# Optimization experiments

Hardware: AMD Instinct MI355X
Metric: run time of the kernel (lower is better)

## Reference

```python
import jax, jax.numpy as jnp
import numpy as np
import math

H, E, HD = 12, 768, 64   # heads, embed_dim, per-head hidden
B, S, L = 8, 512, 512    # batch, dec len, enc len
EPS = 1e-12


def layer_norm(x, w, b):
    u = jnp.mean(x, axis=-1, keepdims=True)
    s = jnp.mean((x - u) ** 2, axis=-1, keepdims=True)
    return w * (x - u) / jnp.sqrt(s + EPS) + b


def gelu(x):
    return x * 0.5 * (1.0 + jax.lax.erf(x / math.sqrt(2.0)))


def attention(k, q, w_k, w_q, pw, pb, mask):
    # k:[b,kl,E] q:[b,ql,E] w_k/w_q:[H,E,HD] mask broadcastable to [b,H,ql,kl]
    kx = jnp.einsum('ble,hed->bhld', k, w_k)
    qx = jnp.einsum('bqe,hed->bhqd', q, w_q)
    score = jnp.einsum('bhqd,bhkd->bhqk', qx, kx) / math.sqrt(HD)
    score = jnp.where(mask, score, jnp.asarray(-1e4, score.dtype))
    attn = jax.nn.softmax(score, axis=-1)
    out = jnp.einsum('bhqk,bhkd->bhqd', attn, kx)  # values are kx (as in source)
    b_, h, ql, d = out.shape
    out = out.transpose(0, 2, 1, 3).reshape(b_, ql, h * d)
    return out @ pw + pb


def setup_inputs() -> dict:
    key = jax.random.key(0)
    ks = jax.random.split(key, 16)
    xav = lambda k, shp, fan: jax.random.normal(k, shp, jnp.float32) * math.sqrt(2.0 / fan)
    inp = {
        'X': jax.random.normal(ks[0], (B, S, E), jnp.float32),
        'enc_outputs': jax.random.normal(ks[1], (B, L, E), jnp.float32),
        'enc_valid_lens': jax.random.randint(ks[2], (B,), 1, L + 1, jnp.int32),
        'w_kx1': xav(ks[3], (H, E, HD), E + HD),
        'w_qx1': xav(ks[4], (H, E, HD), E + HD),
        'proj1_w': xav(ks[5], (H * HD, E), 2 * E),
        'proj1_b': jnp.zeros((E,), jnp.float32),
        'ln1_w': jnp.ones((E,), jnp.float32),
        'ln1_b': jnp.zeros((E,), jnp.float32),
        'w_kx2': xav(ks[6], (H, E, HD), E + HD),
        'w_qx2': xav(ks[7], (H, E, HD), E + HD),
        'proj2_w': xav(ks[8], (H * HD, E), 2 * E),
        'proj2_b': jnp.zeros((E,), jnp.float32),
        'ln2_w': jnp.ones((E,), jnp.float32),
        'ln2_b': jnp.zeros((E,), jnp.float32),
        'ffn_w1': xav(ks[9], (E, E), 2 * E),
        'ffn_b1': jnp.zeros((E,), jnp.float32),
        'ffn_w2': xav(ks[10], (E, E), 2 * E),
        'ffn_b2': jnp.zeros((E,), jnp.float32),
        'ln3_w': jnp.ones((E,), jnp.float32),
        'ln3_b': jnp.zeros((E,), jnp.float32),
    }
    return inp


def reference(X, enc_outputs, enc_valid_lens,
              w_kx1, w_qx1, proj1_w, proj1_b, ln1_w, ln1_b,
              w_kx2, w_qx2, proj2_w, proj2_b, ln2_w, ln2_b,
              ffn_w1, ffn_b1, ffn_w2, ffn_b2, ln3_w, ln3_b):
    s = X.shape[1]
    # training path: dec_valid_lens is 2D -> causal mask in Attention
    causal = jnp.tril(jnp.ones((s, s), dtype=bool))[None, None]          # [1,1,s,s]
    X2 = attention(X, X, w_kx1, w_qx1, proj1_w, proj1_b, causal)
    Y = layer_norm(X2 + X, ln1_w, ln1_b)
    # cross mask: key padding from enc_valid_lens (1D branch)
    kl = enc_outputs.shape[1]
    pad = (jnp.arange(kl)[None] < enc_valid_lens[:, None])[:, None, None]  # [b,1,1,kl]
    Y2 = attention(enc_outputs, Y, w_kx2, w_qx2, proj2_w, proj2_b, pad)
    Z = layer_norm(Y2 + Y, ln2_w, ln2_b)
    F = gelu(Z @ ffn_w1 + ffn_b1) @ ffn_w2 + ffn_b2
    return layer_norm(F + Z, ln3_w, ln3_b)
```

## Files before the change

kernel.cpp:

```cpp
#include <hip/hip_runtime.h>
#include <hip/hip_bf16.h>

typedef __hip_bfloat16 bf16;
typedef __attribute__((ext_vector_type(8))) short s8v;
typedef __attribute__((ext_vector_type(4))) short s4v;
typedef __attribute__((ext_vector_type(4))) float f4v;

#define H_ 12
#define E_ 768
#define HD_ 64
#define B_ 8
#define S_ 512
#define M_ 4096

struct P9 { const void* s[8]; bf16* d[8]; const void* vs[10]; bf16* vd[10]; };

typedef __attribute__((address_space(3))) void lds_void;
typedef const __attribute__((address_space(1))) void g_void;

__device__ __forceinline__ void async_copy16(const bf16* g, short* l) {
    __builtin_amdgcn_global_load_lds((g_void*)g, (lds_void*)l, 16, 0, 0);
}

__device__ __forceinline__ float sh2f(short v) {
    unsigned int u = ((unsigned int)(unsigned short)v) << 16;
    return __uint_as_float(u);
}

__global__ void detect_kernel(const unsigned int* __restrict__ X, int* flag) {
    __shared__ int cnt;
    if (threadIdx.x == 0) cnt = 0;
    __syncthreads();
    int good = 0;
    for (int i = threadIdx.x; i < 16384; i += 256) {
        unsigned e = (X[i] >> 7) & 0xFFu;
        good += (e >= 100u && e <= 141u) ? 1 : 0;
    }
    atomicAdd(&cnt, good);
    __syncthreads();
    if (threadIdx.x == 0) *flag = (cnt > 9830) ? 0 : 1;
}

__global__ void conv2_kernel(const void* s0, const void* s1, bf16* d0, bf16* d1,
                             const int* __restrict__ flag) {
    const int fp32 = *flag;
    const void* s = blockIdx.y ? s1 : s0;
    bf16* d = blockIdx.y ? d1 : d0;
    int i = (blockIdx.x * 256 + threadIdx.x) * 4;
    if (fp32) {
        float4 v = *(const float4*)((const float*)s + i);
        bf16 a = __float2bfloat16(v.x), b = __float2bfloat16(v.y),
             c = __float2bfloat16(v.z), e = __float2bfloat16(v.w);
        s4v o = { *(short*)&a, *(short*)&b, *(short*)&c, *(short*)&e };
        *(s4v*)(d + i) = o;
    } else {
        *(s4v*)(d + i) = *(const s4v*)((const bf16*)s + i);
    }
}

__device__ __forceinline__ bf16 ldcvt(const void* s, int i, int fp32) {
    return fp32 ? __float2bfloat16(((const float*)s)[i]) : ((const bf16*)s)[i];
}

__global__ void repack_kernel(P9 p, const int* __restrict__ flag) {
    const int fp32 = *flag;
    const int z = blockIdx.z;
    if (z == 8) {
        int id = blockIdx.y * 12 + blockIdx.x;
        if (id < 10) {
            const void* s = p.vs[id];
            bf16* d = p.vd[id];
            for (int i = threadIdx.x; i < E_; i += 256) d[i] = ldcvt(s, i, fp32);
        }
        return;
    }
    __shared__ float t[64][65];
    const int c = threadIdx.x & 63, r0 = threadIdx.x >> 6;
    if (z < 4) {
        const void* s = p.s[z];
        bf16* d = p.d[z];
        const int e0 = blockIdx.x * 64, h = blockIdx.y;
        #pragma unroll
        for (int j = 0; j < 16; ++j) {
            int r = r0 * 16 + j;
            int idx = (h * E_ + e0 + r) * HD_ + c;
            t[r][c] = fp32 ? ((const float*)s)[idx] : __bfloat162float(((const bf16*)s)[idx]);
        }
        __syncthreads();
        #pragma unroll
        for (int j = 0; j < 16; ++j) {
            int r = r0 * 16 + j;
            d[(size_t)(h * 64 + r) * E_ + e0 + c] = __float2bfloat16(t[c][r]);
        }
    } else {
        const void* s = p.s[z];
        bf16* d = p.d[z];
        const int k0 = blockIdx.x * 64, n0 = blockIdx.y * 64;
        #pragma unroll
        for (int j = 0; j < 16; ++j) {
            int r = r0 * 16 + j;
            int idx = (k0 + r) * E_ + n0 + c;
            t[r][c] = fp32 ? ((const float*)s)[idx] : __bfloat162float(((const bf16*)s)[idx]);
        }
        __syncthreads();
        #pragma unroll
        for (int j = 0; j < 16; ++j) {
            int r = r0 * 16 + j;
            d[(size_t)(n0 + r) * E_ + k0 + c] = __float2bfloat16(t[c][r]);
        }
    }
}

template <int EPI>
__global__ __launch_bounds__(256, 4) void gemm2(const bf16* __restrict__ A,
                                                const bf16* __restrict__ Bt,
                                                bf16* __restrict__ C,
                                                bf16* __restrict__ C2,
                                                const bf16* __restrict__ bias,
                                                const bf16* __restrict__ res) {
    __shared__ short As[128 * 64];
    __shared__ short Bs[64 * 64];
    const int bm = blockIdx.x, bn = blockIdx.y;
    const int tid = threadIdx.x;
    const int w = tid >> 6, l = tid & 63;
    const int wr = w >> 1, wc = w & 1;
    const int lc = l & 15, quad = l >> 4;
    const int srA = l >> 3, slot = l & 7;

    f4v acc[4][2] = {};

    for (int k0 = 0; k0 < E_; k0 += 64) {
        #pragma unroll
        for (int c = 0; c < 4; ++c) {
            int seg = w * 4 + c;
            int row = seg * 8 + srA;
            int kc = (slot ^ srA) * 8;
            async_copy16(A + (size_t)(bm * 128 + row) * E_ + k0 + kc, &As[seg * 512]);
        }
        #pragma unroll
        for (int c = 0; c < 2; ++c) {
            int seg = w * 2 + c;
            int row = seg * 8 + srA;
            int kc = (slot ^ srA) * 8;
            async_copy16(Bt + (size_t)(bn * 64 + row) * E_ + k0 + kc, &Bs[seg * 512]);
        }
        __syncthreads();

        #pragma unroll
        for (int kk = 0; kk < 2; ++kk) {
            s8v b[2];
            #pragma unroll
            for (int nt = 0; nt < 2; ++nt) {
                int col = wc * 32 + nt * 16 + lc;
                b[nt] = *(const s8v*)&Bs[col * 64 + (((kk * 4 + quad) ^ (col & 7)) * 8)];
            }
            #pragma unroll
            for (int mt = 0; mt < 4; ++mt) {
                int row = wr * 64 + mt * 16 + lc;
                s8v a = *(const s8v*)&As[row * 64 + (((kk * 4 + quad) ^ (row & 7)) * 8)];
                acc[mt][0] = __builtin_amdgcn_mfma_f32_16x16x32_bf16(a, b[0], acc[mt][0], 0, 0, 0);
                acc[mt][1] = __builtin_amdgcn_mfma_f32_16x16x32_bf16(a, b[1], acc[mt][1], 0, 0, 0);
            }
        }
        __syncthreads();
    }

    #pragma unroll
    for (int mt = 0; mt < 4; ++mt)
        #pragma unroll
        for (int nt = 0; nt < 2; ++nt)
            #pragma unroll
            for (int i = 0; i < 4; ++i) {
                int row = bm * 128 + wr * 64 + mt * 16 + quad * 4 + i;
                int col = bn * 64 + wc * 32 + nt * 16 + lc;
                float v = acc[mt][nt][i];
                if (EPI == 3) {
                    if (col < E_) C[(size_t)row * E_ + col] = __float2bfloat16(v);
                    else          C2[(size_t)row * E_ + (col - E_)] = __float2bfloat16(v);
                } else {
                    C[(size_t)row * E_ + col] = __float2bfloat16(v);
                }
            }
}

template <int EPI>
__global__ __launch_bounds__(256, 4) void gemm3(const bf16* __restrict__ A,
                                                const bf16* __restrict__ Bt,
                                                bf16* __restrict__ C,
                                                const bf16* __restrict__ bias,
                                                const bf16* __restrict__ res) {
    __shared__ short As[64 * 64];
    __shared__ short Bs[64 * 64];
    const int bm = blockIdx.x, bn = blockIdx.y;
    const int tid = threadIdx.x;
    const int w = tid >> 6, l = tid & 63;
    const int wr = (w >> 1) * 32, wc = (w & 1) * 32;
    const int lc = l & 15, quad = l >> 4;
    const int srA = l >> 3, slot = l & 7;

    f4v acc[2][2] = {};

    for (int k0 = 0; k0 < E_; k0 += 64) {
        #pragma unroll
        for (int c = 0; c < 2; ++c) {
            int seg = w * 2 + c;
            int row = seg * 8 + srA;
            int kc = (slot ^ srA) * 8;
            async_copy16(A + (size_t)(bm * 64 + row) * E_ + k0 + kc, &As[seg * 512]);
            async_copy16(Bt + (size_t)(bn * 64 + row) * E_ + k0 + kc, &Bs[seg * 512]);
        }
        __syncthreads();

        #pragma unroll
        for (int kk = 0; kk < 2; ++kk) {
            s8v a[2], b[2];
            #pragma unroll
            for (int t = 0; t < 2; ++t) {
                int ar = wr + t * 16 + lc;
                a[t] = *(const s8v*)&As[ar * 64 + (((kk * 4 + quad) ^ (ar & 7)) * 8)];
                int bc = wc + t * 16 + lc;
                b[t] = *(const s8v*)&Bs[bc * 64 + (((kk * 4 + quad) ^ (bc & 7)) * 8)];
            }
            acc[0][0] = __builtin_amdgcn_mfma_f32_16x16x32_bf16(a[0], b[0], acc[0][0], 0, 0, 0);
            acc[0][1] = __builtin_amdgcn_mfma_f32_16x16x32_bf16(a[0], b[1], acc[0][1], 0, 0, 0);
            acc[1][0] = __builtin_amdgcn_mfma_f32_16x16x32_bf16(a[1], b[0], acc[1][0], 0, 0, 0);
            acc[1][1] = __builtin_amdgcn_mfma_f32_16x16x32_bf16(a[1], b[1], acc[1][1], 0, 0, 0);
        }
        __syncthreads();
    }

    #pragma unroll
    for (int mt = 0; mt < 2; ++mt)
        #pragma unroll
        for (int nt = 0; nt < 2; ++nt)
            #pragma unroll
            for (int i = 0; i < 4; ++i) {
                int row = bm * 64 + wr + mt * 16 + quad * 4 + i;
                int col = bn * 64 + wc + nt * 16 + lc;
                float v = acc[mt][nt][i];
                if (EPI == 1)
                    v += __bfloat162float(bias[col]) + __bfloat162float(res[(size_t)row * E_ + col]);
                if (EPI == 2) {
                    v += __bfloat162float(bias[col]);
                    v = 0.5f * v * (1.0f + erff(v * 0.70710678118654752f));
                }
                C[(size_t)row * E_ + col] = __float2bfloat16(v);
            }
}

template <bool CAUSAL>
__global__ __launch_bounds__(256) void attn_kernel(const bf16* __restrict__ Q,
                                                   const bf16* __restrict__ Kx,
                                                   bf16* __restrict__ O,
                                                   const int* __restrict__ vlen) {
    __shared__ short qs[64 * 72];
    __shared__ short ks[64 * 72];
    __shared__ short kts[64 * 72];
    __shared__ short ps[64 * 72];

    const int bh = blockIdx.x;
    const int qt = blockIdx.y;
    const int h = bh % H_, b = bh / H_;
    const int tid = threadIdx.x, w = tid >> 6, l = tid & 63;
    const int lr = (l >> 4) * 4, lc = l & 15, ko = (l >> 4) * 8;

    for (int c = tid * 2; c < tid * 2 + 2; ++c) {
        int row = c >> 3, dc = (c & 7) * 8;
        const bf16* src = Q + (((size_t)(b * S_ + qt * 64 + row) * H_ + h) * HD_ + dc);
        *(s8v*)&qs[row * 72 + dc] = *(const s8v*)src;
    }

    const int valid = CAUSAL ? S_ : vlen[b];
    const int kmax = CAUSAL ? (qt + 1) : ((valid + 63) >> 6);

    float m_i[4], l_i[4];
    for (int i = 0; i < 4; i++) { m_i[i] = -3.0e38f; l_i[i] = 0.0f; }
    f4v o_acc[4] = {};
    __syncthreads();

    for (int kt = 0; kt < kmax; ++kt) {
        for (int c = tid * 2; c < tid * 2 + 2; ++c) {
            int row = c >> 3, dc = (c & 7) * 8;
            const bf16* src = Kx + (((size_t)(b * S_ + kt * 64 + row) * H_ + h) * HD_ + dc);
            s8v v = *(const s8v*)src;
            *(s8v*)&ks[row * 72 + dc] = v;
            #pragma unroll
            for (int j = 0; j < 8; j++) kts[(dc + j) * 72 + row] = v[j];
        }
        __syncthreads();

        f4v sacc[4] = {};
        s8v aq0 = *(const s8v*)&qs[(w * 16 + lc) * 72 + ko];
        s8v aq1 = *(const s8v*)&qs[(w * 16 + lc) * 72 + 32 + ko];
        #pragma unroll
        for (int nt = 0; nt < 4; nt++) {
            s8v bk0 = *(const s8v*)&ks[(nt * 16 + lc) * 72 + ko];
            s8v bk1 = *(const s8v*)&ks[(nt * 16 + lc) * 72 + 32 + ko];
            sacc[nt] = __builtin_amdgcn_mfma_f32_16x16x32_bf16(aq0, bk0, sacc[nt], 0, 0, 0);
            sacc[nt] = __builtin_amdgcn_mfma_f32_16x16x32_bf16(aq1, bk1, sacc[nt], 0, 0, 0);
        }

        #pragma unroll
        for (int i = 0; i < 4; i++) {
            int qabs = qt * 64 + w * 16 + lr + i;
            float sv[4];
            float mx = -3.0e38f;
            #pragma unroll
            for (int nt = 0; nt < 4; nt++) {
                int kabs = kt * 64 + nt * 16 + lc;
                float s = sacc[nt][i] * 0.125f;
                bool ok = CAUSAL ? (kabs <= qabs) : (kabs < valid);
                sv[nt] = ok ? s : -1.0e4f;
                mx = fmaxf(mx, sv[nt]);
            }
            #pragma unroll
            for (int off = 1; off < 16; off <<= 1) mx = fmaxf(mx, __shfl_xor(mx, off));
            float mnew = fmaxf(m_i[i], mx);
            float alpha = __expf(m_i[i] - mnew);
            float psum = 0.0f;
            #pragma unroll
            for (int nt = 0; nt < 4; nt++) {
                float p = __expf(sv[nt] - mnew);
                psum += p;
                *(bf16*)&ps[(w * 16 + lr + i) * 72 + nt * 16 + lc] = __float2bfloat16(p);
            }
            #pragma unroll
            for (int off = 1; off < 16; off <<= 1) psum += __shfl_xor(psum, off);
            l_i[i] = l_i[i] * alpha + psum;
            m_i[i] = mnew;
            #pragma unroll
            for (int dt = 0; dt < 4; dt++) o_acc[dt][i] *= alpha;
        }
        __syncthreads();

        s8v ap0 = *(const s8v*)&ps[(w * 16 + lc) * 72 + ko];
        s8v ap1 = *(const s8v*)&ps[(w * 16 + lc) * 72 + 32 + ko];
        #pragma unroll
        for (int dt = 0; dt < 4; dt++) {
            s8v bv0 = *(const s8v*)&kts[(dt * 16 + lc) * 72 + ko];
            s8v bv1 = *(const s8v*)&kts[(dt * 16 + lc) * 72 + 32 + ko];
            o_acc[dt] = __builtin_amdgcn_mfma_f32_16x16x32_bf16(ap0, bv0, o_acc[dt], 0, 0, 0);
            o_acc[dt] = __builtin_amdgcn_mfma_f32_16x16x32_bf16(ap1, bv1, o_acc[dt], 0, 0, 0);
        }
        __syncthreads();
    }

    #pragma unroll
    for (int dt = 0; dt < 4; dt++)
        #pragma unroll
        for (int i = 0; i < 4; i++) {
            int q = qt * 64 + w * 16 + lr + i;
            int d = dt * 16 + lc;
            float v = o_acc[dt][i] / l_i[i];
            O[((size_t)(b * S_ + q) * H_ + h) * HD_ + d] = __float2bfloat16(v);
        }
}

__global__ __launch_bounds__(256) void ln2_kernel(const bf16* __restrict__ X,
                                                  const bf16* __restrict__ wv,
                                                  const bf16* __restrict__ bv,
                                                  bf16* __restrict__ outb,
                                                  float* __restrict__ outf,
                                                  const int* __restrict__ flag) {
    const int row = blockIdx.x * 4 + (threadIdx.x >> 6);
    const int l = threadIdx.x & 63;
    const bf16* xr = X + (size_t)row * E_;
    s8v v8 = *(const s8v*)(xr + l * 8);
    s4v v4 = *(const s4v*)(xr + 512 + l * 4);
    float x[12];
    #pragma unroll
    for (int j = 0; j < 8; ++j) x[j] = sh2f(v8[j]);
    #pragma unroll
    for (int j = 0; j < 4; ++j) x[8 + j] = sh2f(v4[j]);
    float s = 0.f, ss = 0.f;
    #pragma unroll
    for (int j = 0; j < 12; ++j) { s += x[j]; ss += x[j] * x[j]; }
    #pragma unroll
    for (int off = 1; off < 64; off <<= 1) {
        s += __shfl_xor(s, off);
        ss += __shfl_xor(ss, off);
    }
    float mu = s * (1.0f / E_);
    float var = ss * (1.0f / E_) - mu * mu;
    float rstd = rsqrtf(fmaxf(var, 0.0f) + 1e-12f);
    const bool f32out = (outf != nullptr) && (*flag != 0);
    #pragma unroll
    for (int j = 0; j < 12; ++j) {
        int c = (j < 8) ? (l * 8 + j) : (512 + l * 4 + (j - 8));
        float v = (x[j] - mu) * rstd * __bfloat162float(wv[c]) + __bfloat162float(bv[c]);
        if (f32out) outf[(size_t)row * E_ + c] = v;
        else        outb[(size_t)row * E_ + c] = __float2bfloat16(v);
    }
}

extern "C" void kernel_launch(void* const* d_in, const int* in_sizes, int n_in,
                              void* d_out, int out_size, void* d_ws, size_t ws_size,
                              hipStream_t stream) {
    const void* X = d_in[0];
    const void* enc = d_in[1];
    const int* vlen = (const int*)d_in[2];

    char* ws = (char*)d_ws;
    int* flag = (int*)ws;
    bf16* vecs = (bf16*)(ws + 256);
    char* wbase = ws + 16384;
    const size_t WSZ = (size_t)E_ * E_ * sizeof(bf16);
    bf16* wk1 = (bf16*)(wbase + 0 * WSZ);
    bf16* wq1 = (bf16*)(wbase + 1 * WSZ);
    bf16* wk2 = (bf16*)(wbase + 2 * WSZ);
    bf16* wq2 = (bf16*)(wbase + 3 * WSZ);
    bf16* p1t = (bf16*)(wbase + 4 * WSZ);
    bf16* p2t = (bf16*)(wbase + 5 * WSZ);
    bf16* f1t = (bf16*)(wbase + 6 * WSZ);
    bf16* f2t = (bf16*)(wbase + 7 * WSZ);
    const size_t ASZ = (size_t)M_ * E_ * sizeof(bf16);
    char* abase = wbase + 8 * WSZ;
    bf16* Xc   = (bf16*)(abase + 0 * ASZ);
    bf16* ENCc = (bf16*)(abase + 1 * ASZ);
    bf16* A0 = (bf16*)(abase + 2 * ASZ);
    bf16* A1 = (bf16*)(abase + 3 * ASZ);
    bf16* A2 = (bf16*)(abase + 4 * ASZ);
    bf16* A3 = (bf16*)(abase + 5 * ASZ);

    bf16* bias1 = vecs + 0 * E_;
    bf16* lw1   = vecs + 1 * E_;
    bf16* lb1   = vecs + 2 * E_;
    bf16* bias2 = vecs + 3 * E_;
    bf16* lw2   = vecs + 4 * E_;
    bf16* lb2   = vecs + 5 * E_;
    bf16* fb1   = vecs + 6 * E_;
    bf16* fb2   = vecs + 7 * E_;
    bf16* lw3   = vecs + 8 * E_;
    bf16* lb3   = vecs + 9 * E_;

    detect_kernel<<<1, 256, 0, stream>>>((const unsigned int*)X, flag);

    conv2_kernel<<<dim3(M_ * E_ / 1024, 2), 256, 0, stream>>>(X, enc, Xc, ENCc, flag);

    P9 rp;
    rp.s[0] = d_in[3];  rp.d[0] = wk1;
    rp.s[1] = d_in[4];  rp.d[1] = wq1;
    rp.s[2] = d_in[9];  rp.d[2] = wk2;
    rp.s[3] = d_in[10]; rp.d[3] = wq2;
    rp.s[4] = d_in[5];  rp.d[4] = p1t;
    rp.s[5] = d_in[11]; rp.d[5] = p2t;
    rp.s[6] = d_in[15]; rp.d[6] = f1t;
    rp.s[7] = d_in[17]; rp.d[7] = f2t;
    rp.vs[0] = d_in[6];  rp.vd[0] = bias1;
    rp.vs[1] = d_in[7];  rp.vd[1] = lw1;
    rp.vs[2] = d_in[8];  rp.vd[2] = lb1;
    rp.vs[3] = d_in[12]; rp.vd[3] = bias2;
    rp.vs[4] = d_in[13]; rp.vd[4] = lw2;
    rp.vs[5] = d_in[14]; rp.vd[5] = lb2;
    rp.vs[6] = d_in[16]; rp.vd[6] = fb1;
    rp.vs[7] = d_in[18]; rp.vd[7] = fb2;
    rp.vs[8] = d_in[19]; rp.vd[8] = lw3;
    rp.vs[9] = d_in[20]; rp.vd[9] = lb3;
    repack_kernel<<<dim3(12, 12, 9), 256, 0, stream>>>(rp, flag);

    gemm2<3><<<dim3(32, 24), 256, 0, stream>>>(Xc, wk1, A0, A1, nullptr, nullptr);
    attn_kernel<true><<<dim3(96, 8), 256, 0, stream>>>(A1, A0, A2, nullptr);
    gemm3<1><<<dim3(64, 12), 256, 0, stream>>>(A2, p1t, A3, bias1, Xc);
    ln2_kernel<<<M_ / 4, 256, 0, stream>>>(A3, lw1, lb1, A0, nullptr, flag);
    gemm3<0><<<dim3(64, 12), 256, 0, stream>>>(ENCc, wk2, A1, nullptr, nullptr);
    gemm3<0><<<dim3(64, 12), 256, 0, stream>>>(A0, wq2, A2, nullptr, nullptr);
    attn_kernel<false><<<dim3(96, 8), 256, 0, stream>>>(A2, A1, A3, vlen);
    gemm3<1><<<dim3(64, 12), 256, 0, stream>>>(A3, p2t, A1, bias2, A0);
    ln2_kernel<<<M_ / 4, 256, 0, stream>>>(A1, lw2, lb2, A2, nullptr, flag);
    gemm3<2><<<dim3(64, 12), 256, 0, stream>>>(A2, f1t, A3, fb1, nullptr);
    gemm3<1><<<dim3(64, 12), 256, 0, stream>>>(A3, f2t, A1, fb2, A2);
    ln2_kernel<<<M_ / 4, 256, 0, stream>>>(A1, lw3, lb3, (bf16*)d_out, (float*)d_out, flag);
}
```

Before: 303.6 us.

## Fuse K/Q projections into one GEMM, pre-transpose K, async-load attention tiles

Replaces gemm2/gemm3 with a single 64x96-tile gemm4. The EPI=3 variant computes layer-1 K, Q and the layer-2 encoder K projection in one launch by picking an alternate A input for the high column blocks. A new ktrans kernel writes transposed K for both attentions ahead of time. The attention kernel then loads Q, K and K^T with async global-to-LDS copies into XOR-swizzled tiles instead of transposing through scalar LDS stores, and drops two barriers. This cuts launch count and the in-loop transpose cost, at the price of extra workspace, an extra transpose pass, and reliance on the barrier ordering around the ps buffer.

Measured after the change: 316.5 us. 4.2% more time.

```diff
diff --git a/kernel.cpp b/kernel.cpp
--- a/kernel.cpp
+++ b/kernel.cpp
@@ -111,132 +111,108 @@
     }
 }
 
+__global__ void ktrans_kernel(const bf16* __restrict__ K1, const bf16* __restrict__ K2,
+                              bf16* __restrict__ KT1, bf16* __restrict__ KT2) {
+    __shared__ short t[64 * 72];
+    const bf16* src = blockIdx.z ? K2 : K1;
+    bf16* dst = blockIdx.z ? KT2 : KT1;
+    const int s0 = blockIdx.x * 64, bh = blockIdx.y;
+    const int b = bh / H_, h = bh % H_;
+    const int tid = threadIdx.x;
+    #pragma unroll
+    for (int it = 0; it < 2; ++it) {
+        int idx = tid * 2 + it;
+        int row = idx >> 3, ch = (idx & 7) * 8;
+        s8v v = *(const s8v*)(src + ((size_t)(b * S_ + s0 + row) * H_ + h) * HD_ + ch);
+        *(s8v*)&t[row * 72 + ch] = v;
+    }
+    __syncthreads();
+    const int orow = tid >> 2, oc = (tid & 3) * 16;
+    s8v o0, o1;
+    #pragma unroll
+    for (int j = 0; j < 8; ++j) o0[j] = t[(oc + j) * 72 + orow];
+    #pragma unroll
+    for (int j = 0; j < 8; ++j) o1[j] = t[(oc + 8 + j) * 72 + orow];
+    bf16* dp = dst + (size_t)(bh * 64 + orow) * S_ + s0 + oc;
+    *(s8v*)dp = o0;
+    *(s8v*)(dp + 8) = o1;
+}
+
 template <int EPI>
-__global__ __launch_bounds__(256, 4) void gemm2(const bf16* __restrict__ A,
+__global__ __launch_bounds__(256, 4) void gemm4(const bf16* __restrict__ A,
+                                                const bf16* __restrict__ Aalt,
                                                 const bf16* __restrict__ Bt,
                                                 bf16* __restrict__ C,
                                                 bf16* __restrict__ C2,
+                                                bf16* __restrict__ C3,
                                                 const bf16* __restrict__ bias,
                                                 const bf16* __restrict__ res) {
-    __shared__ short As[128 * 64];
-    __shared__ short Bs[64 * 64];
+    __shared__ short As[64 * 64];
+    __shared__ short Bs[96 * 64];
     const int bm = blockIdx.x, bn = blockIdx.y;
     const int tid = threadIdx.x;
     const int w = tid >> 6, l = tid & 63;
-    const int wr = w >> 1, wc = w & 1;
+    const int wr = (w >> 1) * 32, wc = (w & 1) * 48;
     const int lc = l & 15, quad = l >> 4;
     const int srA = l >> 3, slot = l & 7;
-
-    f4v acc[4][2] = {};
+    const int kc = (slot ^ srA) * 8;
+
+    const bf16* Ap = (EPI == 3 && bn >= 16) ? Aalt : A;
+
+    f4v acc[2][3] = {};
 
     for (int k0 = 0; k0 < E_; k0 += 64) {
         #pragma unroll
-        for (int c = 0; c < 4; ++c) {
-            int seg = w * 4 + c;
-            int row = seg * 8 + srA;
-            int kc = (slot ^ srA) * 8;
-            async_copy16(A + (size_t)(bm * 128 + row) * E_ + k0 + kc, &As[seg * 512]);
-        }
-        #pragma unroll
-        for (int c = 0; c < 2; ++c) {
-            int seg = w * 2 + c;
-            int row = seg * 8 + srA;
-            int kc = (slot ^ srA) * 8;
-            async_copy16(Bt + (size_t)(bn * 64 + row) * E_ + k0 + kc, &Bs[seg * 512]);
+        for (int c = 0; c < 5; ++c) {
+            int seg = w * 5 + c;
+            if (seg < 8) {
+                int row = seg * 8 + srA;
+                async_copy16(Ap + (size_t)(bm * 64 + row) * E_ + k0 + kc, &As[seg * 512]);
+            } else {
+                int row = (seg - 8) * 8 + srA;
+                async_copy16(Bt + (size_t)(bn * 96 + row) * E_ + k0 + kc, &Bs[(seg - 8) * 512]);
+            }
         }
         __syncthreads();
 
         #pragma unroll
         for (int kk = 0; kk < 2; ++kk) {
-            s8v b[2];
-            #pragma unroll
-            for (int nt = 0; nt < 2; ++nt) {
-                int col = wc * 32 + nt * 16 + lc;
-                b[nt] = *(const s8v*)&Bs[col * 64 + (((kk * 4 + quad) ^ (col & 7)) * 8)];
-            }
-            #pragma unroll
-            for (int mt = 0; mt < 4; ++mt) {
-                int row = wr * 64 + mt * 16 + lc;
-                s8v a = *(const s8v*)&As[row * 64 + (((kk * 4 + quad) ^ (row & 7)) * 8)];
-                acc[mt][0] = __builtin_amdgcn_mfma_f32_16x16x32_bf16(a, b[0], acc[mt][0], 0, 0, 0);
-                acc[mt][1] = __builtin_amdgcn_mfma_f32_16x16x32_bf16(a, b[1], acc[mt][1], 0, 0, 0);
-            }
-        }
-        __syncthreads();
-    }
-
-    #pragma unroll
-    for (int mt = 0; mt < 4; ++mt)
-        #pragma unroll
-        for (int nt = 0; nt < 2; ++nt)
-            #pragma unroll
-            for (int i = 0; i < 4; ++i) {
-                int row = bm * 128 + wr * 64 + mt * 16 + quad * 4 + i;
-                int col = bn * 64 + wc * 32 + nt * 16 + lc;
-                float v = acc[mt][nt][i];
-                if (EPI == 3) {
-                    if (col < E_) C[(size_t)row * E_ + col] = __float2bfloat16(v);
-                    else          C2[(size_t)row * E_ + (col - E_)] = __float2bfloat16(v);
-                } else {
-                    C[(size_t)row * E_ + col] = __float2bfloat16(v);
-                }
-            }
-}
-
-template <int EPI>
-__global__ __launch_bounds__(256, 4) void gemm3(const bf16* __restrict__ A,
-                                                const bf16* __restrict__ Bt,
-                                                bf16* __restrict__ C,
-                                                const bf16* __restrict__ bias,
-                                                const bf16* __restrict__ res) {
-    __shared__ short As[64 * 64];
-    __shared__ short Bs[64 * 64];
-    const int bm = blockIdx.x, bn = blockIdx.y;
-    const int tid = threadIdx.x;
-    const int w = tid >> 6, l = tid & 63;
-    const int wr = (w >> 1) * 32, wc = (w & 1) * 32;
-    const int lc = l & 15, quad = l >> 4;
-    const int srA = l >> 3, slot = l & 7;
-
-    f4v acc[2][2] = {};
-
-    for (int k0 = 0; k0 < E_; k0 += 64) {
-        #pragma unroll
-        for (int c = 0; c < 2; ++c) {
-            int seg = w * 2 + c;
-            int row = seg * 8 + srA;
-            int kc = (slot ^ srA) * 8;
-            async_copy16(A + (size_t)(bm * 64 + row) * E_ + k0 + kc, &As[seg * 512]);
-            async_copy16(Bt + (size_t)(bn * 64 + row) * E_ + k0 + kc, &Bs[seg * 512]);
-        }
-        __syncthreads();
-
-        #pragma unroll
-        for (int kk = 0; kk < 2; ++kk) {
-            s8v a[2], b[2];
+            s8v a[2], b[3];
             #pragma unroll
             for (int t = 0; t < 2; ++t) {
                 int ar = wr + t * 16 + lc;
                 a[t] = *(const s8v*)&As[ar * 64 + (((kk * 4 + quad) ^ (ar & 7)) * 8)];
+            }
+            #pragma unroll
+            for (int t = 0; t < 3; ++t) {
                 int bc = wc + t * 16 + lc;
                 b[t] = *(const s8v*)&Bs[bc * 64 + (((kk * 4 + quad) ^ (bc & 7)) * 8)];
             }
-            acc[0][0] = __builtin_amdgcn_mfma_f32_16x16x32_bf16(a[0], b[0], acc[0][0], 0, 0, 0);
-            acc[0][1] = __builtin_amdgcn_mfma_f32_16x16x32_bf16(a[0], b[1], acc[0][1], 0, 0, 0);
-            acc[1][0] = __builtin_amdgcn_mfma_f32_16x16x32_bf16(a[1], b[0], acc[1][0], 0, 0, 0);
-            acc[1][1] = __builtin_amdgcn_mfma_f32_16x16x32_bf16(a[1], b[1], acc[1][1], 0, 0, 0);
-        }
-        __syncthreads();
+            #pragma unroll
+            for (int mt = 0; mt < 2; ++mt)
+                #pragma unroll
+                for (int nt = 0; nt < 3; ++nt)
+                    acc[mt][nt] = __builtin_amdgcn_mfma_f32_16x16x32_bf16(a[mt], b[nt], acc[mt][nt], 0, 0, 0);
+        }
+        __syncthreads();
+    }
+
+    bf16* Co = C;
+    int coff = 0;
+    if (EPI == 3) {
+        if (bn < 8)       { Co = C;  coff = 0; }
+        else if (bn < 16) { Co = C2; coff = 768; }
+        else              { Co = C3; coff = 1536; }
     }
 
     #pragma unroll
     for (int mt = 0; mt < 2; ++mt)
         #pragma unroll
-        for (int nt = 0; nt < 2; ++nt)
+        for (int nt = 0; nt < 3; ++nt)
             #pragma unroll
             for (int i = 0; i < 4; ++i) {
                 int row = bm * 64 + wr + mt * 16 + quad * 4 + i;
-                int col = bn * 64 + wc + nt * 16 + lc;
+                int col = bn * 96 + wc + nt * 16 + lc;
                 float v = acc[mt][nt][i];
                 if (EPI == 1)
                     v += __bfloat162float(bias[col]) + __bfloat162float(res[(size_t)row * E_ + col]);
@@ -244,30 +220,34 @@
                     v += __bfloat162float(bias[col]);
                     v = 0.5f * v * (1.0f + erff(v * 0.70710678118654752f));
                 }
-                C[(size_t)row * E_ + col] = __float2bfloat16(v);
+                if (EPI == 3) Co[(size_t)row * E_ + (col - coff)] = __float2bfloat16(v);
+                else          C[(size_t)row * E_ + col] = __float2bfloat16(v);
             }
 }
 
 template <bool CAUSAL>
 __global__ __launch_bounds__(256) void attn_kernel(const bf16* __restrict__ Q,
                                                    const bf16* __restrict__ Kx,
+                                                   const bf16* __restrict__ KT,
                                                    bf16* __restrict__ O,
                                                    const int* __restrict__ vlen) {
-    __shared__ short qs[64 * 72];
-    __shared__ short ks[64 * 72];
-    __shared__ short kts[64 * 72];
+    __shared__ short qs[64 * 64];
+    __shared__ short ks[64 * 64];
+    __shared__ short kts[64 * 64];
     __shared__ short ps[64 * 72];
 
-    const int bh = blockIdx.x;
-    const int qt = blockIdx.y;
+    const int bh = blockIdx.x, qt = blockIdx.y;
     const int h = bh % H_, b = bh / H_;
     const int tid = threadIdx.x, w = tid >> 6, l = tid & 63;
-    const int lr = (l >> 4) * 4, lc = l & 15, ko = (l >> 4) * 8;
-
-    for (int c = tid * 2; c < tid * 2 + 2; ++c) {
-        int row = c >> 3, dc = (c & 7) * 8;
-        const bf16* src = Q + (((size_t)(b * S_ + qt * 64 + row) * H_ + h) * HD_ + dc);
-        *(s8v*)&qs[row * 72 + dc] = *(const s8v*)src;
+    const int lr = (l >> 4) * 4, lc = l & 15, quad = l >> 4;
+    const int srA = l >> 3, slot = l & 7;
+    const int kc = (slot ^ srA) * 8;
+
+    #pragma unroll
+    for (int c = 0; c < 2; ++c) {
+        int seg = w * 2 + c;
+        int row = seg * 8 + srA;
+        async_copy16(Q + ((size_t)(b * S_ + qt * 64 + row) * H_ + h) * HD_ + kc, &qs[seg * 512]);
     }
 
     const int valid = CAUSAL ? S_ : vlen[b];
@@ -276,26 +256,26 @@
     float m_i[4], l_i[4];
     for (int i = 0; i < 4; i++) { m_i[i] = -3.0e38f; l_i[i] = 0.0f; }
     f4v o_acc[4] = {};
-    __syncthreads();
 
     for (int kt = 0; kt < kmax; ++kt) {
-        for (int c = tid * 2; c < tid * 2 + 2; ++c) {
-            int row = c >> 3, dc = (c & 7) * 8;
-            const bf16* src = Kx + (((size_t)(b * S_ + kt * 64 + row) * H_ + h) * HD_ + dc);
-            s8v v = *(const s8v*)src;
-            *(s8v*)&ks[row * 72 + dc] = v;
-            #pragma unroll
-            for (int j = 0; j < 8; j++) kts[(dc + j) * 72 + row] = v[j];
+        #pragma unroll
+        for (int c = 0; c < 2; ++c) {
+            int seg = w * 2 + c;
+            int row = seg * 8 + srA;
+            async_copy16(Kx + ((size_t)(b * S_ + kt * 64 + row) * H_ + h) * HD_ + kc, &ks[seg * 512]);
+            async_copy16(KT + (size_t)(bh * 64 + row) * S_ + kt * 64 + kc, &kts[seg * 512]);
         }
         __syncthreads();
 
         f4v sacc[4] = {};
-        s8v aq0 = *(const s8v*)&qs[(w * 16 + lc) * 72 + ko];
-        s8v aq1 = *(const s8v*)&qs[(w * 16 + lc) * 72 + 32 + ko];
+        const int rq = w * 16 + lc;
+        s8v aq0 = *(const s8v*)&qs[rq * 64 + ((quad ^ (rq & 7)) * 8)];
+        s8v aq1 = *(const s8v*)&qs[rq * 64 + (((4 + quad) ^ (rq & 7)) * 8)];
         #pragma unroll
         for (int nt = 0; nt < 4; nt++) {
-            s8v bk0 = *(const s8v*)&ks[(nt * 16 + lc) * 72 + ko];
-            s8v bk1 = *(const s8v*)&ks[(nt * 16 + lc) * 72 + 32 + ko];
+            int rk = nt * 16 + lc;
+            s8v bk0 = *(const s8v*)&ks[rk * 64 + ((quad ^ (rk & 7)) * 8)];
+            s8v bk1 = *(const s8v*)&ks[rk * 64 + (((4 + quad) ^ (rk & 7)) * 8)];
             sacc[nt] = __builtin_amdgcn_mfma_f32_16x16x32_bf16(aq0, bk0, sacc[nt], 0, 0, 0);
             sacc[nt] = __builtin_amdgcn_mfma_f32_16x16x32_bf16(aq1, bk1, sacc[nt], 0, 0, 0);
         }
@@ -331,14 +311,14 @@
             #pragma unroll
             for (int dt = 0; dt < 4; dt++) o_acc[dt][i] *= alpha;
         }
-        __syncthreads();
-
-        s8v ap0 = *(const s8v*)&ps[(w * 16 + lc) * 72 + ko];
-        s8v ap1 = *(const s8v*)&ps[(w * 16 + lc) * 72 + 32 + ko];
+
+        s8v ap0 = *(const s8v*)&ps[rq * 72 + quad * 8];
+        s8v ap1 = *(const s8v*)&ps[rq * 72 + 32 + quad * 8];
         #pragma unroll
         for (int dt = 0; dt < 4; dt++) {
-            s8v bv0 = *(const s8v*)&kts[(dt * 16 + lc) * 72 + ko];
-            s8v bv1 = *(const s8v*)&kts[(dt * 16 + lc) * 72 + 32 + ko];
+            int rd = dt * 16 + lc;
+            s8v bv0 = *(const s8v*)&kts[rd * 64 + ((quad ^ (rd & 7)) * 8)];
+            s8v bv1 = *(const s8v*)&kts[rd * 64 + (((4 + quad) ^ (rd & 7)) * 8)];
             o_acc[dt] = __builtin_amdgcn_mfma_f32_16x16x32_bf16(ap0, bv0, o_acc[dt], 0, 0, 0);
             o_acc[dt] = __builtin_amdgcn_mfma_f32_16x16x32_bf16(ap1, bv1, o_acc[dt], 0, 0, 0);
         }
@@ -417,10 +397,14 @@
     char* abase = wbase + 8 * WSZ;
     bf16* Xc   = (bf16*)(abase + 0 * ASZ);
     bf16* ENCc = (bf16*)(abase + 1 * ASZ);
-    bf16* A0 = (bf16*)(abase + 2 * ASZ);
-    bf16* A1 = (bf16*)(abase + 3 * ASZ);
-    bf16* A2 = (bf16*)(abase + 4 * ASZ);
-    bf16* A3 = (bf16*)(abase + 5 * ASZ);
+    bf16* A0  = (bf16*)(abase + 2 * ASZ);
+    bf16* A1  = (bf16*)(abase + 3 * ASZ);
+    bf16* A2  = (bf16*)(abase + 4 * ASZ);
+    bf16* A3  = (bf16*)(abase + 5 * ASZ);
+    bf16* A4  = (bf16*)(abase + 6 * ASZ);
+    bf16* A5  = (bf16*)(abase + 7 * ASZ);
+    bf16* KT1 = (bf16*)(abase + 8 * ASZ);
+    bf16* KT2 = (bf16*)(abase + 9 * ASZ);
 
     bf16* bias1 = vecs + 0 * E_;
     bf16* lw1   = vecs + 1 * E_;
@@ -434,7 +418,6 @@
     bf16* lb3   = vecs + 9 * E_;
 
     detect_kernel<<<1, 256, 0, stream>>>((const unsigned int*)X, flag);
-
     conv2_kernel<<<dim3(M_ * E_ / 1024, 2), 256, 0, stream>>>(X, enc, Xc, ENCc, flag);
 
     P9 rp;
@@ -458,16 +441,19 @@
     rp.vs[9] = d_in[20]; rp.vd[9] = lb3;
     repack_kernel<<<dim3(12, 12, 9), 256, 0, stream>>>(rp, flag);
 
-    gemm2<3><<<dim3(32, 24), 256, 0, stream>>>(Xc, wk1, A0, A1, nullptr, nullptr);
-    attn_kernel<true><<<dim3(96, 8), 256, 0, stream>>>(A1, A0, A2, nullptr);
-    gemm3<1><<<dim3(64, 12), 256, 0, stream>>>(A2, p1t, A3, bias1, Xc);
-    ln2_kernel<<<M_ / 4, 256, 0, stream>>>(A3, lw1, lb1, A0, nullptr, flag);
-    gemm3<0><<<dim3(64, 12), 256, 0, stream>>>(ENCc, wk2, A1, nullptr, nullptr);
-    gemm3<0><<<dim3(64, 12), 256, 0, stream>>>(A0, wq2, A2, nullptr, nullptr);
-    attn_kernel<false><<<dim3(96, 8), 256, 0, stream>>>(A2, A1, A3, vlen);
-    gemm3<1><<<dim3(64, 12), 256, 0, stream>>>(A3, p2t, A1, bias2, A0);
-    ln2_kernel<<<M_ / 4, 256, 0, stream>>>(A1, lw2, lb2, A2, nullptr, flag);
-    gemm3<2><<<dim3(64, 12), 256, 0, stream>>>(A2, f1t, A3, fb1, nullptr);
-    gemm3<1><<<dim3(64, 12), 256, 0, stream>>>(A3, f2t, A1, fb2, A2);
-    ln2_kernel<<<M_ / 4, 256, 0, stream>>>(A1, lw3, lb3, (bf16*)d_out, (float*)d_out, flag);
-}
+    gemm4<3><<<dim3(64, 24), 256, 0, stream>>>(Xc, ENCc, wk1, A0, A1, A4, nullptr, nullptr);
+    ktrans_kernel<<<dim3(8, 96, 2), 256, 0, stream>>>(A0, A4, KT1, KT2);
+
+    attn_kernel<true><<<dim3(96, 8), 256, 0, stream>>>(A1, A0, KT1, A2, nullptr);
+    gemm4<1><<<dim3(64, 8), 256, 0, stream>>>(A2, nullptr, p1t, A3, nullptr, nullptr, bias1, Xc);
+    ln2_kernel<<<M_ / 4, 256, 0, stream>>>(A3, lw1, lb1, A5, nullptr, flag);
+
+    gemm4<0><<<dim3(64, 8), 256, 0, stream>>>(A5, nullptr, wq2, A1, nullptr, nullptr, nullptr, nullptr);
+    attn_kernel<false><<<dim3(96, 8), 256, 0, stream>>>(A1, A4, KT2, A2, vlen);
+    gemm4<1><<<dim3(64, 8), 256, 0, stream>>>(A2, nullptr, p2t, A3, nullptr, nullptr, bias2, A5);
+    ln2_kernel<<<M_ / 4, 256, 0, stream>>>(A3, lw2, lb2, A0, nullptr, flag);
+
+    gemm4<2><<<dim3(64, 8), 256, 0, stream>>>(A0, nullptr, f1t, A1, nullptr, nullptr, fb1, nullptr);
+    gemm4<1><<<dim3(64, 8), 256, 0, stream>>>(A1, nullptr, f2t, A2, nullptr, nullptr, fb2, A0);
+    ln2_kernel<<<M_ / 4, 256, 0, stream>>>(A2, lw3, lb3, (bf16*)d_out, (float*)d_out, flag);
+}
```
